# Kernel optimization log

Hardware: AMD Instinct MI355X
Metric: run time of the kernel (lower is better)

The kernel has to match this reference:

```python
import jax, jax.numpy as jnp
import numpy as np

D = 1024
H = 16
HD = D // H
COND = 128
MLP = 4 * D
B, S = 4, 1024
LN_EPS = 1e-5


def _layer_norm(x, w):
    # fp32 LayerNorm (no bias), then scale by weight, matching custom LayerNorm
    xf = x.astype(jnp.float32)
    mu = jnp.mean(xf, axis=-1, keepdims=True)
    var = jnp.mean(jnp.square(xf - mu), axis=-1, keepdims=True)
    y = (xf - mu) * jax.lax.rsqrt(var + LN_EPS)
    return y * w[None, None, :]


def _modulate(x, shift, scale):
    # shift/scale: [B, D] -> broadcast over seq
    return x * (1.0 + scale[:, None, :]) + shift[:, None, :]


def _rope(t, cos, sin):
    # t: [B,S,H,hd]; cos/sin: [S, hd//2]  (GPT-NeoX half-split rotary)
    c = cos[None, :, None, :]
    s = sin[None, :, None, :]
    t1, t2 = jnp.split(t, 2, axis=-1)
    return jnp.concatenate([t1 * c - t2 * s, t2 * c + t1 * s], axis=-1)


def setup_inputs() -> dict:
    key = jax.random.key(0)
    ks = jax.random.split(key, 12)
    std = 0.02
    inp = {
        "x": jax.random.normal(ks[0], (B, S, D), dtype=jnp.float32),
        "c": jax.random.normal(ks[1], (B, COND), dtype=jnp.float32),
        "norm1_w": jnp.ones((D,), dtype=jnp.float32),
        "norm2_w": jnp.ones((D,), dtype=jnp.float32),
        "w_qkv": jax.random.normal(ks[2], (D, 3 * D), dtype=jnp.float32) * std,
        "w_out": jax.random.normal(ks[3], (D, D), dtype=jnp.float32) * std,
        "w1": jax.random.normal(ks[4], (D, MLP), dtype=jnp.float32) * std,
        "b1": jnp.zeros((MLP,), dtype=jnp.float32),
        "w2": jax.random.normal(ks[5], (MLP, D), dtype=jnp.float32) * std,
        "b2": jnp.zeros((D,), dtype=jnp.float32),
        "adaLN_w": jax.random.normal(ks[6], (COND, 6 * D), dtype=jnp.float32) * std,
        "adaLN_b": jnp.zeros((6 * D,), dtype=jnp.float32),
    }
    # rotary tables: cos/sin [S, hd//2]
    inv_freq = 1.0 / (10000.0 ** (jnp.arange(0, HD, 2, dtype=jnp.float32) / HD))
    t = jnp.arange(S, dtype=jnp.float32)
    freqs = t[:, None] * inv_freq[None, :]  # [S, hd//2]
    inp["cos"] = jnp.cos(freqs)
    inp["sin"] = jnp.sin(freqs)
    return inp


def reference(x, c, norm1_w, norm2_w, w_qkv, w_out, w1, b1, w2, b2, adaLN_w, adaLN_b, cos, sin):
    b, s, d = x.shape
    hd = 2 * cos.shape[-1]
    h = d // hd

    # adaLN modulation -> 6 chunks of [B, D]
    mod = c @ adaLN_w + adaLN_b
    shift_msa, scale_msa, gate_msa, shift_mlp, scale_mlp, gate_mlp = jnp.split(mod, 6, axis=-1)

    x_skip = x
    xm = _modulate(_layer_norm(x, norm1_w), shift_msa, scale_msa)

    qkv = (xm @ w_qkv).reshape(b, s, 3, h, hd)
    q = _rope(qkv[:, :, 0], cos, sin)
    k = _rope(qkv[:, :, 1], cos, sin)
    v = qkv[:, :, 2]

    scale = 1.0 / jnp.sqrt(jnp.asarray(hd, dtype=x.dtype))
    scores = jnp.einsum("bshd,bthd->bhst", q, k) * scale
    probs = jax.nn.softmax(scores, axis=-1)
    attn = jnp.einsum("bhst,bthd->bshd", probs, v).reshape(b, s, d)

    # bias_dropout_add_scale (inference: dropout off): residual + gate * out
    x = x_skip + gate_msa[:, None, :] * (attn @ w_out)

    xm2 = _modulate(_layer_norm(x, norm2_w), shift_mlp, scale_mlp)
    hdn = jax.nn.gelu(xm2 @ w1 + b1, approximate=True)
    mlp_out = hdn @ w2 + b2
    x = x + gate_mlp[:, None, :] * mlp_out
    return x
```

## Files before the change

kernel.cpp:

```cpp
#include <hip/hip_runtime.h>

typedef unsigned short u16;
typedef unsigned int u32;
typedef short bf16x8 __attribute__((ext_vector_type(8)));
typedef float f32x4 __attribute__((ext_vector_type(4)));

#define DD 1024
#define SS 1024
#define HH 16
#define HDIM 64
#define MODW 6144

__device__ __forceinline__ float b2f(u16 h){ u32 u = ((u32)h)<<16; return __builtin_bit_cast(float,u); }
__device__ __forceinline__ u16 f2b(float f){
  u32 u = __builtin_bit_cast(u32,f);
  return (u16)((u + 0x7fffu + ((u>>16)&1u))>>16);
}
__device__ __forceinline__ void gload16(const u16* g, u16* l){
  __builtin_amdgcn_global_load_lds((const __attribute__((address_space(1))) void*)g,
                                   (__attribute__((address_space(3))) void*)l, 16, 0, 0);
}

__global__ void k_zero(float* __restrict__ out){
  int i = blockIdx.x*256 + threadIdx.x;
  ((float4*)out)[i] = make_float4(0.f,0.f,0.f,0.f);
}

__device__ __forceinline__ void tcast_tile(const float* in, u16* out, int K, int N, int bx, int by){
  __shared__ float t[32][33];
  int n0 = bx*32, k0 = by*32;
  int tx = threadIdx.x & 31, ty = threadIdx.x >> 5;
  #pragma unroll
  for (int i=0;i<4;i++){
    int k = k0 + ty + i*8;
    t[ty+i*8][tx] = in[(size_t)k*N + n0 + tx];
  }
  __syncthreads();
  #pragma unroll
  for (int i=0;i<4;i++){
    int n = n0 + ty + i*8;
    out[(size_t)n*K + k0 + tx] = f2b(t[tx][ty+i*8]);
  }
}
__global__ void k_prep(const float* __restrict__ wqkv, const float* __restrict__ wout,
                       const float* __restrict__ w1, const float* __restrict__ w2,
                       u16* __restrict__ wqkvT, u16* __restrict__ woutT,
                       u16* __restrict__ w1T, u16* __restrict__ w2T,
                       const float* __restrict__ c, const float* __restrict__ aw,
                       const float* __restrict__ ab, float* __restrict__ mod){
  int bid = blockIdx.x;
  if (bid < 3072)       tcast_tile(wqkv, wqkvT, 1024, 3072, bid%96,  bid/96);
  else if (bid < 4096){ int t=bid-3072; tcast_tile(wout, woutT, 1024, 1024, t%32, t/32); }
  else if (bid < 8192){ int t=bid-4096; tcast_tile(w1,   w1T,   1024, 4096, t%128,t/128); }
  else if (bid < 12288){int t=bid-8192; tcast_tile(w2,   w2T,   4096, 1024, t%32, t/32); }
  else {
    int t = bid - 12288;
    int n = (t%24)*256 + threadIdx.x;
    int bb = t/24;
    float acc = ab[n];
    #pragma unroll 4
    for (int k=0;k<128;k++) acc += c[bb*128+k]*aw[(size_t)k*MODW + n];
    mod[(size_t)bb*MODW + n] = acc;
  }
}

__global__ void k_ln_mod(const float* __restrict__ x, const float* __restrict__ w,
                         const float* __restrict__ mod, int shc, int scc,
                         u16* __restrict__ out){
  int row = blockIdx.x;
  int b = row >> 10;
  const float* xr = x + (size_t)row*DD;
  float4 v = ((const float4*)xr)[threadIdx.x];
  float s = v.x+v.y+v.z+v.w;
  float sq = v.x*v.x+v.y*v.y+v.z*v.z+v.w*v.w;
  #pragma unroll
  for (int o=32;o;o>>=1){ s += __shfl_xor(s,o); sq += __shfl_xor(sq,o); }
  __shared__ float ls[4], lq[4];
  int wid = threadIdx.x>>6, lane = threadIdx.x&63;
  if (lane==0){ ls[wid]=s; lq[wid]=sq; }
  __syncthreads();
  s = ls[0]+ls[1]+ls[2]+ls[3]; sq = lq[0]+lq[1]+lq[2]+lq[3];
  float mu = s*(1.f/DD);
  float var = sq*(1.f/DD) - mu*mu;
  float rs = rsqrtf(var + 1e-5f);
  int d0 = threadIdx.x*4;
  const float* mb = mod + (size_t)b*MODW;
  float y0 = ((v.x-mu)*rs*w[d0+0])*(1.f+mb[scc+d0+0]) + mb[shc+d0+0];
  float y1 = ((v.y-mu)*rs*w[d0+1])*(1.f+mb[scc+d0+1]) + mb[shc+d0+1];
  float y2 = ((v.z-mu)*rs*w[d0+2])*(1.f+mb[scc+d0+2]) + mb[shc+d0+2];
  float y3 = ((v.w-mu)*rs*w[d0+3])*(1.f+mb[scc+d0+3]) + mb[shc+d0+3];
  uint2 pk;
  pk.x = (u32)f2b(y0) | ((u32)f2b(y1)<<16);
  pk.y = (u32)f2b(y2) | ((u32)f2b(y3)<<16);
  ((uint2*)(out + (size_t)row*DD))[threadIdx.x] = pk;
}

enum { EPI_QKV=0, EPI_GELU=2, EPI_PARTB=5 };

template<int EPI>
__launch_bounds__(512, 2)
__global__ void k_gemm256(const u16* __restrict__ A, const u16* __restrict__ Bt,
                          int M, int N, int K, int kstride,
                          const float* __restrict__ bias,
                          u16* __restrict__ outb,
                          const float* __restrict__ cosb, const float* __restrict__ sinb,
                          u16* __restrict__ qh, u16* __restrict__ kh, u16* __restrict__ vt){
  __shared__ __align__(16) u16 lds[4][2][8192];
  int tid = threadIdx.x, lane = tid & 63;
  int wid = tid >> 6, wr = wid >> 2, wc = wid & 3;
  int bm = blockIdx.x*256, bn = blockIdx.y*256, z = blockIdx.z;
  f32x4 acc[8][4] = {};
  int srow = (tid>>6)*16 + (tid&15);
  int skk  = ((tid>>4)&3)*8;
  const u16* pa = A  + (size_t)(bm+srow)*kstride + (size_t)z*K + skk;
  const u16* pb = Bt + (size_t)(bn+srow)*kstride + (size_t)z*K + skk;
  size_t rh = (size_t)128*kstride;
  int nk = K >> 5;
  #pragma unroll
  for (int t=0; t<3; ++t){
    gload16(pa + t*32,      &lds[t][0][tid*8]);
    gload16(pa + rh + t*32, &lds[t][0][4096 + tid*8]);
    gload16(pb + t*32,      &lds[t][1][tid*8]);
    gload16(pb + rh + t*32, &lds[t][1][4096 + tid*8]);
  }
  for (int t=0; t<nk; ++t){
    const u16* lA = &lds[t&3][0][0];
    const u16* lB = &lds[t&3][1][0];
    int ahead = nk-1-t;
    if (ahead >= 2)      asm volatile("s_waitcnt vmcnt(8)" ::: "memory");
    else if (ahead == 1) asm volatile("s_waitcnt vmcnt(4)" ::: "memory");
    else                 asm volatile("s_waitcnt vmcnt(0)" ::: "memory");
    __builtin_amdgcn_s_barrier();
    if (t+3 < nk){
      int u = t+3;
      gload16(pa + u*32,      &lds[u&3][0][tid*8]);
      gload16(pa + rh + u*32, &lds[u&3][0][4096 + tid*8]);
      gload16(pb + u*32,      &lds[u&3][1][tid*8]);
      gload16(pb + rh + u*32, &lds[u&3][1][4096 + tid*8]);
    }
    bf16x8 fa[8], fb[4];
    #pragma unroll
    for (int mi=0;mi<8;mi++) fa[mi] = *(const bf16x8*)(lA + ((wr*8+mi)*64 + lane)*8);
    #pragma unroll
    for (int ni=0;ni<4;ni++) fb[ni] = *(const bf16x8*)(lB + ((wc*4+ni)*64 + lane)*8);
    asm volatile("s_waitcnt lgkmcnt(0)" ::: "memory");
    __builtin_amdgcn_sched_barrier(0);
    __builtin_amdgcn_s_setprio(1);
    #pragma unroll
    for (int mi=0;mi<8;mi++)
      #pragma unroll
      for (int ni=0;ni<4;ni++)
        acc[mi][ni] = __builtin_amdgcn_mfma_f32_16x16x32_bf16(fa[mi], fb[ni], acc[mi][ni], 0,0,0);
    __builtin_amdgcn_s_setprio(0);
  }
  int ln = lane & 15;
  int rbase = bm + wr*128 + ((lane>>4)<<2);
  if (EPI == EPI_QKV){
    int cbg = bn + wc*64;
    int ii = cbg >> 10;
    int hh = (cbg >> 6) & 15;
    if (ii == 2){
      #pragma unroll
      for (int mi=0;mi<8;mi++){
        int row = rbase + mi*16;
        int s = row & 1023, b = row >> 10;
        size_t ob = (size_t)(b*16+hh)*65536;
        #pragma unroll
        for (int ni=0;ni<4;ni++){
          int d = ni*16 + ln;
          u32 lo = (u32)f2b(acc[mi][ni][0]) | ((u32)f2b(acc[mi][ni][1])<<16);
          u32 hi = (u32)f2b(acc[mi][ni][2]) | ((u32)f2b(acc[mi][ni][3])<<16);
          *(uint2*)(vt + ob + (size_t)d*1024 + s) = make_uint2(lo,hi);
        }
      }
    } else {
      u16* dst = (ii==0) ? qh : kh;
      #pragma unroll
      for (int mi=0;mi<8;mi++){
        #pragma unroll
        for (int r=0;r<4;r++){
          int row = rbase + mi*16 + r;
          int s = row & 1023, b = row >> 10;
          size_t ob = ((size_t)(b*16+hh)*1024 + s)*64;
          #pragma unroll
          for (int ni=0;ni<2;ni++){
            int dlow = ni*16 + ln;
            float cc = cosb[s*32 + dlow], sn = sinb[s*32 + dlow];
            float t1 = acc[mi][ni][r], t2 = acc[mi][ni+2][r];
            dst[ob + dlow]      = f2b(t1*cc - t2*sn);
            dst[ob + dlow + 32] = f2b(t2*cc + t1*sn);
          }
        }
      }
    }
    return;
  }
  if (EPI == EPI_PARTB){
    u16* po = outb + (size_t)z*M*N;
    #pragma unroll
    for (int mi=0;mi<8;mi++)
      #pragma unroll
      for (int ni=0;ni<4;ni++){
        int col = bn + wc*64 + ni*16 + ln;
        #pragma unroll
        for (int r=0;r<4;r++)
          po[(size_t)(rbase+mi*16+r)*N + col] = f2b(acc[mi][ni][r]);
      }
    return;
  }
  #pragma unroll
  for (int mi=0;mi<8;mi++)
    #pragma unroll
    for (int ni=0;ni<4;ni++){
      int col = bn + wc*64 + ni*16 + ln;
      float bb = bias[col];
      #pragma unroll
      for (int r=0;r<4;r++){
        float t = acc[mi][ni][r] + bb;
        float y = 0.7978845608f*(t + 0.044715f*t*t*t);
        y = fminf(fmaxf(y, -15.f), 15.f);
        float e = __expf(2.f*y);
        float g = 0.5f*t*(1.f + (e-1.f)/(e+1.f));
        outb[(size_t)(rbase+mi*16+r)*N + col] = f2b(g);
      }
    }
}

__global__ void k_red_ln(const u16* __restrict__ part, const float* __restrict__ x,
                         const float* __restrict__ mod, const float* __restrict__ w,
                         float* __restrict__ x2, u16* __restrict__ act){
  int row = blockIdx.x;
  int b = row >> 10;
  int tid = threadIdx.x;
  int col = tid*4;
  size_t base = (size_t)row*DD + col;
  const size_t MN = (size_t)4096*1024;
  uint2 p0 = *(const uint2*)(part + base);
  uint2 p1 = *(const uint2*)(part + MN + base);
  const float* mb = mod + (size_t)b*MODW;
  float4 g = *(const float4*)(mb + 2*DD + col);
  float4 rr = *(const float4*)(x + base);
  float4 v;
  v.x = rr.x + g.x*(b2f((u16)p0.x)      + b2f((u16)p1.x));
  v.y = rr.y + g.y*(b2f((u16)(p0.x>>16))+ b2f((u16)(p1.x>>16)));
  v.z = rr.z + g.z*(b2f((u16)p0.y)      + b2f((u16)p1.y));
  v.w = rr.w + g.w*(b2f((u16)(p0.y>>16))+ b2f((u16)(p1.y>>16)));
  *(float4*)(x2 + base) = v;
  float s = v.x+v.y+v.z+v.w;
  float sq = v.x*v.x+v.y*v.y+v.z*v.z+v.w*v.w;
  #pragma unroll
  for (int o=32;o;o>>=1){ s += __shfl_xor(s,o); sq += __shfl_xor(sq,o); }
  __shared__ float ls[4], lq[4];
  int wid = tid>>6, lane = tid&63;
  if (lane==0){ ls[wid]=s; lq[wid]=sq; }
  __syncthreads();
  s = ls[0]+ls[1]+ls[2]+ls[3]; sq = lq[0]+lq[1]+lq[2]+lq[3];
  float mu = s*(1.f/DD);
  float var = sq*(1.f/DD) - mu*mu;
  float rs = rsqrtf(var + 1e-5f);
  float y0 = ((v.x-mu)*rs*w[col+0])*(1.f+mb[4*DD+col+0]) + mb[3*DD+col+0];
  float y1 = ((v.y-mu)*rs*w[col+1])*(1.f+mb[4*DD+col+1]) + mb[3*DD+col+1];
  float y2 = ((v.z-mu)*rs*w[col+2])*(1.f+mb[4*DD+col+2]) + mb[3*DD+col+2];
  float y3 = ((v.w-mu)*rs*w[col+3])*(1.f+mb[4*DD+col+3]) + mb[3*DD+col+3];
  uint2 pk;
  pk.x = (u32)f2b(y0) | ((u32)f2b(y1)<<16);
  pk.y = (u32)f2b(y2) | ((u32)f2b(y3)<<16);
  *(uint2*)(act + base) = pk;
}

__global__ void k_reduce4b(const u16* __restrict__ part, size_t MN,
                           const float* __restrict__ resid,
                           const float* __restrict__ mod, int gate_off,
                           const float* __restrict__ bias,
                           float* __restrict__ out){
  int i = blockIdx.x*256 + threadIdx.x;
  int e = i<<2;
  int col = e & 1023;
  int row = e >> 10;
  int b = row >> 10;
  float4 s = make_float4(0.f,0.f,0.f,0.f);
  #pragma unroll
  for (int z=0; z<4; z++){
    uint2 p = ((const uint2*)(part + (size_t)z*MN))[i];
    s.x += b2f((u16)p.x); s.y += b2f((u16)(p.x>>16));
    s.z += b2f((u16)p.y); s.w += b2f((u16)(p.y>>16));
  }
  float4 bb = *(const float4*)(bias + col);
  s.x+=bb.x; s.y+=bb.y; s.z+=bb.z; s.w+=bb.w;
  float4 g = *(const float4*)(mod + (size_t)b*MODW + gate_off + col);
  float4 rr = ((const float4*)resid)[i];
  float4 o;
  o.x = rr.x + g.x*s.x; o.y = rr.y + g.y*s.y;
  o.z = rr.z + g.z*s.z; o.w = rr.w + g.w*s.w;
  ((float4*)out)[i] = o;
}

__launch_bounds__(256)
__global__ void k_attn(const u16* __restrict__ qh, const u16* __restrict__ kh,
                       const u16* __restrict__ vt, u16* __restrict__ attn){
  int blk = blockIdx.x;
  int bh = blk >> 4;
  int qt = blk & 15;
  int tid = threadIdx.x, lane = tid&63, wid = tid>>6;
  int ln = lane&15, kg = lane>>4;
  __shared__ __align__(16) u16 Ks[64*72];
  __shared__ __align__(16) u16 Vs[64*72];
  __shared__ __align__(16) float ps[4][16*72];
  const size_t hb = (size_t)bh*SS*HDIM;

  int qrow = qt*64 + wid*16 + ln;
  const u16* qp = qh + hb + (size_t)qrow*64 + kg*8;
  bf16x8 qf0 = *(const bf16x8*)qp;
  bf16x8 qf1 = *(const bf16x8*)(qp + 32);

  float m[4], l[4];
  f32x4 oc[4] = {};
  #pragma unroll
  for (int r=0;r<4;r++){ m[r]=-1e30f; l[r]=0.f; }
  float* psw = ps[wid];

  for (int kt=0; kt<16; ++kt){
    __syncthreads();
    {
      int row = tid>>2, c = tid&3;
      const u16* gk = kh + hb + (size_t)(kt*64+row)*64 + c*16;
      *(uint4*)(Ks + row*72 + c*16)     = *(const uint4*)gk;
      *(uint4*)(Ks + row*72 + c*16 + 8) = *(const uint4*)(gk+8);
      const u16* gv = vt + hb + (size_t)row*1024 + kt*64 + c*16;
      *(uint4*)(Vs + row*72 + c*16)     = *(const uint4*)gv;
      *(uint4*)(Vs + row*72 + c*16 + 8) = *(const uint4*)(gv+8);
    }
    __syncthreads();

    f32x4 sc[4] = {};
    #pragma unroll
    for (int c=0;c<4;c++){
      bf16x8 kf0 = *(const bf16x8*)(Ks + (c*16+ln)*72 + kg*8);
      bf16x8 kf1 = *(const bf16x8*)(Ks + (c*16+ln)*72 + kg*8 + 32);
      sc[c] = __builtin_amdgcn_mfma_f32_16x16x32_bf16(qf0, kf0, sc[c], 0,0,0);
      sc[c] = __builtin_amdgcn_mfma_f32_16x16x32_bf16(qf1, kf1, sc[c], 0,0,0);
    }
    #pragma unroll
    for (int r=0;r<4;r++){
      float s0 = sc[0][r]*0.125f, s1 = sc[1][r]*0.125f;
      float s2 = sc[2][r]*0.125f, s3 = sc[3][r]*0.125f;
      float mx = fmaxf(fmaxf(s0,s1), fmaxf(s2,s3));
      #pragma unroll
      for (int off=8;off;off>>=1) mx = fmaxf(mx, __shfl_xor(mx, off));
      float mn = fmaxf(m[r], mx);
      float al = __expf(m[r]-mn);
      m[r] = mn;
      float p0=__expf(s0-mn), p1=__expf(s1-mn), p2=__expf(s2-mn), p3=__expf(s3-mn);
      float sum = (p0+p1)+(p2+p3);
      #pragma unroll
      for (int off=8;off;off>>=1) sum += __shfl_xor(sum, off);
      l[r] = l[r]*al + sum;
      #pragma unroll
      for (int c=0;c<4;c++) oc[c][r] *= al;
      int ro = (kg*4+r)*72;
      psw[ro +  0 + ln] = p0;
      psw[ro + 16 + ln] = p1;
      psw[ro + 32 + ln] = p2;
      psw[ro + 48 + ln] = p3;
    }
    #pragma unroll
    for (int kc=0; kc<2; ++kc){
      const float* pr = psw + ln*72 + kg*8 + kc*32;
      f32x4 a0 = *(const f32x4*)pr;
      f32x4 a1 = *(const f32x4*)(pr+4);
      bf16x8 af;
      af[0]=f2b(a0[0]); af[1]=f2b(a0[1]); af[2]=f2b(a0[2]); af[3]=f2b(a0[3]);
      af[4]=f2b(a1[0]); af[5]=f2b(a1[1]); af[6]=f2b(a1[2]); af[7]=f2b(a1[3]);
      #pragma unroll
      for (int c=0;c<4;c++){
        bf16x8 vf = *(const bf16x8*)(Vs + (c*16+ln)*72 + kg*8 + kc*32);
        oc[c] = __builtin_amdgcn_mfma_f32_16x16x32_bf16(af, vf, oc[c], 0,0,0);
      }
    }
  }
  int b = bh >> 4, h = bh & 15;
  #pragma unroll
  for (int r=0;r<4;r++){
    int srow = qt*64 + wid*16 + kg*4 + r;
    float inv = 1.f/l[r];
    u16* op = attn + (size_t)(b*1024+srow)*DD + h*64;
    #pragma unroll
    for (int c=0;c<4;c++) op[c*16+ln] = f2b(oc[c][r]*inv);
  }
}

extern "C" void kernel_launch(void* const* d_in, const int* in_sizes, int n_in,
                              void* d_out, int out_size, void* d_ws, size_t ws_size,
                              hipStream_t stream){
  const float* x   = (const float*)d_in[0];
  const float* c   = (const float*)d_in[1];
  const float* n1w = (const float*)d_in[2];
  const float* n2w = (const float*)d_in[3];
  const float* wqkv= (const float*)d_in[4];
  const float* wout= (const float*)d_in[5];
  const float* w1  = (const float*)d_in[6];
  const float* b1  = (const float*)d_in[7];
  const float* w2  = (const float*)d_in[8];
  const float* b2  = (const float*)d_in[9];
  const float* aw  = (const float*)d_in[10];
  const float* ab  = (const float*)d_in[11];
  const float* cosb= (const float*)d_in[12];
  const float* sinb= (const float*)d_in[13];

  const size_t REQ = 117538816;
  if (ws_size < REQ){
    k_zero<<<4096,256,0,stream>>>((float*)d_out);
    return;
  }
  char* ws = (char*)d_ws;
  u16*   wqkvT = (u16*)(ws + 0);
  u16*   woutT = (u16*)(ws + 6291456);
  u16*   act   = (u16*)(ws + 8388608);
  float* mod   = (float*)(ws + 16777216);
  float* x2    = (float*)(ws + 16875520);
  u16*   qh    = (u16*)(ws + 16875520);
  u16*   kh    = (u16*)(ws + 25264128);
  u16*   vt    = (u16*)(ws + 33652736);
  u16*   part2b= (u16*)(ws + 33652736);
  u16*   hbuf  = (u16*)(ws + 33652736);
  u16*   w1T   = (u16*)(ws + 67207168);
  u16*   w2T   = (u16*)(ws + 75595776);
  u16*   part4b= (u16*)(ws + 83984384);

  k_prep<<<12384,256,0,stream>>>(wqkv, wout, w1, w2, wqkvT, woutT, w1T, w2T, c, aw, ab, mod);
  k_ln_mod<<<4096,256,0,stream>>>(x, n1w, mod, 0*DD, 1*DD, act);
  k_gemm256<EPI_QKV ><<<dim3(16,12,1),512,0,stream>>>(act, wqkvT, 4096,3072,1024,1024,
        nullptr, nullptr, cosb, sinb, qh, kh, vt);
  k_attn<<<1024,256,0,stream>>>(qh, kh, vt, act);
  k_gemm256<EPI_PARTB><<<dim3(16,4,2),512,0,stream>>>(act, woutT, 4096,1024,512,1024,
        nullptr, part2b, nullptr, nullptr, nullptr, nullptr, nullptr);
  k_red_ln<<<4096,256,0,stream>>>(part2b, x, mod, n2w, x2, act);
  k_gemm256<EPI_GELU><<<dim3(16,16,1),512,0,stream>>>(act, w1T, 4096,4096,1024,1024,
        b1, hbuf, nullptr, nullptr, nullptr, nullptr, nullptr);
  k_gemm256<EPI_PARTB><<<dim3(16,4,4),512,0,stream>>>(hbuf, w2T, 4096,1024,1024,4096,
        nullptr, part4b, nullptr, nullptr, nullptr, nullptr, nullptr);
  k_reduce4b<<<4096,256,0,stream>>>(part4b, (size_t)4096*1024, x2, mod, 5*DD, b2, (float*)d_out);
}
```

Baseline: 377.5 us.

## Double-buffer attention K/V via async LDS loads and keep P in registers

Rewrites the attention inner loop to prefetch the next K/V tile into a second LDS buffer using global_load_lds with XOR-swizzled layout, overlapping loads with compute. The QK^T operands are swapped so each lane owns a query column, which removes the per-row shuffle reductions and the fp32 LDS round trip for probabilities. P is packed to bf16 with the hardware pack-convert instruction and redistributed by shuffles instead. The softmax scale is folded into Q in the QKV epilogue, and the attention kernel now requests an occupancy hint. This adds shuffle traffic and hand-placed waitcnt/barrier logic that must stay correct.

```diff
diff --git a/kernel.cpp b/kernel.cpp
--- a/kernel.cpp
+++ b/kernel.cpp
@@ -15,6 +15,9 @@
 __device__ __forceinline__ u16 f2b(float f){
   u32 u = __builtin_bit_cast(u32,f);
   return (u16)((u + 0x7fffu + ((u>>16)&1u))>>16);
+}
+__device__ __forceinline__ u32 cvtpk(float a, float b){
+  u32 r; asm("v_cvt_pk_bf16_f32 %0, %1, %2" : "=v"(r) : "v"(a), "v"(b)); return r;
 }
 __device__ __forceinline__ void gload16(const u16* g, u16* l){
   __builtin_amdgcn_global_load_lds((const __attribute__((address_space(1))) void*)g,
@@ -175,6 +178,7 @@
       }
     } else {
       u16* dst = (ii==0) ? qh : kh;
+      float qs = (ii==0) ? 0.125f : 1.0f;
       #pragma unroll
       for (int mi=0;mi<8;mi++){
         #pragma unroll
@@ -187,8 +191,8 @@
             int dlow = ni*16 + ln;
             float cc = cosb[s*32 + dlow], sn = sinb[s*32 + dlow];
             float t1 = acc[mi][ni][r], t2 = acc[mi][ni+2][r];
-            dst[ob + dlow]      = f2b(t1*cc - t2*sn);
-            dst[ob + dlow + 32] = f2b(t2*cc + t1*sn);
+            dst[ob + dlow]      = f2b((t1*cc - t2*sn)*qs);
+            dst[ob + dlow + 32] = f2b((t2*cc + t1*sn)*qs);
           }
         }
       }
@@ -295,7 +299,7 @@
   ((float4*)out)[i] = o;
 }
 
-__launch_bounds__(256)
+__launch_bounds__(256, 4)
 __global__ void k_attn(const u16* __restrict__ qh, const u16* __restrict__ kh,
                        const u16* __restrict__ vt, u16* __restrict__ attn){
   int blk = blockIdx.x;
@@ -303,9 +307,8 @@
   int qt = blk & 15;
   int tid = threadIdx.x, lane = tid&63, wid = tid>>6;
   int ln = lane&15, kg = lane>>4;
-  __shared__ __align__(16) u16 Ks[64*72];
-  __shared__ __align__(16) u16 Vs[64*72];
-  __shared__ __align__(16) float ps[4][16*72];
+  int sw = ln & 7;
+  __shared__ __align__(16) u16 KV[2][2][4096];
   const size_t hb = (size_t)bh*SS*HDIM;
 
   int qrow = qt*64 + wid*16 + ln;
@@ -313,79 +316,105 @@
   bf16x8 qf0 = *(const bf16x8*)qp;
   bf16x8 qf1 = *(const bf16x8*)(qp + 32);
 
-  float m[4], l[4];
+  int w0i = wid*64 + lane, w1i = w0i + 256;
+  int r0 = w0i>>3, sl0 = (w0i&7) ^ (r0&7);
+  int r1 = w1i>>3, sl1 = (w1i&7) ^ (r1&7);
+  const u16* gk0 = kh + hb + (size_t)r0*64 + sl0*8;
+  const u16* gk1 = kh + hb + (size_t)r1*64 + sl1*8;
+  const u16* gv0 = vt + hb + (size_t)r0*1024 + sl0*8;
+  const u16* gv1 = vt + hb + (size_t)r1*1024 + sl1*8;
+
+  float mrun = -1e30f, lrun = 0.f;
   f32x4 oc[4] = {};
-  #pragma unroll
-  for (int r=0;r<4;r++){ m[r]=-1e30f; l[r]=0.f; }
-  float* psw = ps[wid];
+
+  gload16(gk0, &KV[0][0][w0i*8]);
+  gload16(gk1, &KV[0][0][w1i*8]);
+  gload16(gv0, &KV[0][1][w0i*8]);
+  gload16(gv1, &KV[0][1][w1i*8]);
 
   for (int kt=0; kt<16; ++kt){
-    __syncthreads();
-    {
-      int row = tid>>2, c = tid&3;
-      const u16* gk = kh + hb + (size_t)(kt*64+row)*64 + c*16;
-      *(uint4*)(Ks + row*72 + c*16)     = *(const uint4*)gk;
-      *(uint4*)(Ks + row*72 + c*16 + 8) = *(const uint4*)(gk+8);
-      const u16* gv = vt + hb + (size_t)row*1024 + kt*64 + c*16;
-      *(uint4*)(Vs + row*72 + c*16)     = *(const uint4*)gv;
-      *(uint4*)(Vs + row*72 + c*16 + 8) = *(const uint4*)(gv+8);
-    }
-    __syncthreads();
-
-    f32x4 sc[4] = {};
+    int buf = kt & 1;
+    __builtin_amdgcn_s_barrier();
+    asm volatile("" ::: "memory");
+    if (kt < 15){
+      int u = kt+1;
+      gload16(gk0 + u*4096, &KV[buf^1][0][w0i*8]);
+      gload16(gk1 + u*4096, &KV[buf^1][0][w1i*8]);
+      gload16(gv0 + u*64,   &KV[buf^1][1][w0i*8]);
+      gload16(gv1 + u*64,   &KV[buf^1][1][w1i*8]);
+      asm volatile("s_waitcnt vmcnt(4)" ::: "memory");
+    } else {
+      asm volatile("s_waitcnt vmcnt(0)" ::: "memory");
+    }
+    __builtin_amdgcn_s_barrier();
+    const u16* Kb = KV[buf][0];
+    const u16* Vb = KV[buf][1];
+
+    f32x4 sc[4];
     #pragma unroll
     for (int c=0;c<4;c++){
-      bf16x8 kf0 = *(const bf16x8*)(Ks + (c*16+ln)*72 + kg*8);
-      bf16x8 kf1 = *(const bf16x8*)(Ks + (c*16+ln)*72 + kg*8 + 32);
-      sc[c] = __builtin_amdgcn_mfma_f32_16x16x32_bf16(qf0, kf0, sc[c], 0,0,0);
-      sc[c] = __builtin_amdgcn_mfma_f32_16x16x32_bf16(qf1, kf1, sc[c], 0,0,0);
-    }
-    #pragma unroll
-    for (int r=0;r<4;r++){
-      float s0 = sc[0][r]*0.125f, s1 = sc[1][r]*0.125f;
-      float s2 = sc[2][r]*0.125f, s3 = sc[3][r]*0.125f;
-      float mx = fmaxf(fmaxf(s0,s1), fmaxf(s2,s3));
-      #pragma unroll
-      for (int off=8;off;off>>=1) mx = fmaxf(mx, __shfl_xor(mx, off));
-      float mn = fmaxf(m[r], mx);
-      float al = __expf(m[r]-mn);
-      m[r] = mn;
-      float p0=__expf(s0-mn), p1=__expf(s1-mn), p2=__expf(s2-mn), p3=__expf(s3-mn);
-      float sum = (p0+p1)+(p2+p3);
-      #pragma unroll
-      for (int off=8;off;off>>=1) sum += __shfl_xor(sum, off);
-      l[r] = l[r]*al + sum;
-      #pragma unroll
-      for (int c=0;c<4;c++) oc[c][r] *= al;
-      int ro = (kg*4+r)*72;
-      psw[ro +  0 + ln] = p0;
-      psw[ro + 16 + ln] = p1;
-      psw[ro + 32 + ln] = p2;
-      psw[ro + 48 + ln] = p3;
-    }
-    #pragma unroll
-    for (int kc=0; kc<2; ++kc){
-      const float* pr = psw + ln*72 + kg*8 + kc*32;
-      f32x4 a0 = *(const f32x4*)pr;
-      f32x4 a1 = *(const f32x4*)(pr+4);
-      bf16x8 af;
-      af[0]=f2b(a0[0]); af[1]=f2b(a0[1]); af[2]=f2b(a0[2]); af[3]=f2b(a0[3]);
-      af[4]=f2b(a1[0]); af[5]=f2b(a1[1]); af[6]=f2b(a1[2]); af[7]=f2b(a1[3]);
+      const u16* kr = Kb + (c*16+ln)*64;
+      bf16x8 kf0 = *(const bf16x8*)(kr + (((kg  )^sw)<<3));
+      bf16x8 kf1 = *(const bf16x8*)(kr + (((kg+4)^sw)<<3));
+      f32x4 zz = {};
+      zz   = __builtin_amdgcn_mfma_f32_16x16x32_bf16(kf0, qf0, zz, 0,0,0);
+      sc[c]= __builtin_amdgcn_mfma_f32_16x16x32_bf16(kf1, qf1, zz, 0,0,0);
+    }
+    float mx = fmaxf(fmaxf(fmaxf(sc[0][0],sc[0][1]),fmaxf(sc[0][2],sc[0][3])),
+                     fmaxf(fmaxf(sc[1][0],sc[1][1]),fmaxf(sc[1][2],sc[1][3])));
+    float mx2= fmaxf(fmaxf(fmaxf(sc[2][0],sc[2][1]),fmaxf(sc[2][2],sc[2][3])),
+                     fmaxf(fmaxf(sc[3][0],sc[3][1]),fmaxf(sc[3][2],sc[3][3])));
+    mx = fmaxf(mx, mx2);
+    mx = fmaxf(mx, __shfl_xor(mx, 16));
+    mx = fmaxf(mx, __shfl_xor(mx, 32));
+    float mn = fmaxf(mrun, mx);
+    float al = __expf(mrun - mn);
+    mrun = mn;
+    u32 pk[4][2];
+    float sum = 0.f;
+    #pragma unroll
+    for (int c=0;c<4;c++){
+      float p0 = __expf(sc[c][0]-mn), p1 = __expf(sc[c][1]-mn);
+      float p2 = __expf(sc[c][2]-mn), p3 = __expf(sc[c][3]-mn);
+      sum += (p0+p1)+(p2+p3);
+      pk[c][0] = cvtpk(p0,p1);
+      pk[c][1] = cvtpk(p2,p3);
+    }
+    sum += __shfl_xor(sum, 16);
+    sum += __shfl_xor(sum, 32);
+    lrun = lrun*al + sum;
+    float alr0 = __shfl(al, kg*4+0), alr1 = __shfl(al, kg*4+1);
+    float alr2 = __shfl(al, kg*4+2), alr3 = __shfl(al, kg*4+3);
+    #pragma unroll
+    for (int c=0;c<4;c++){ oc[c][0]*=alr0; oc[c][1]*=alr1; oc[c][2]*=alr2; oc[c][3]*=alr3; }
+    int srcA = ((kg&1)<<5) + ln;
+    int hi = kg >> 1;
+    #pragma unroll
+    for (int kc=0;kc<2;kc++){
+      u32 a0 = (u32)__shfl((int)pk[2*kc  ][0], srcA   ), b0 = (u32)__shfl((int)pk[2*kc+1][0], srcA   );
+      u32 a1 = (u32)__shfl((int)pk[2*kc  ][1], srcA   ), b1 = (u32)__shfl((int)pk[2*kc+1][1], srcA   );
+      u32 a2 = (u32)__shfl((int)pk[2*kc  ][0], srcA+16), b2 = (u32)__shfl((int)pk[2*kc+1][0], srcA+16);
+      u32 a3 = (u32)__shfl((int)pk[2*kc  ][1], srcA+16), b3 = (u32)__shfl((int)pk[2*kc+1][1], srcA+16);
+      uint4 wv = make_uint4(hi? b0:a0, hi? b1:a1, hi? b2:a2, hi? b3:a3);
+      bf16x8 af = __builtin_bit_cast(bf16x8, wv);
       #pragma unroll
       for (int c=0;c<4;c++){
-        bf16x8 vf = *(const bf16x8*)(Vs + (c*16+ln)*72 + kg*8 + kc*32);
+        const u16* vr = Vb + (c*16+ln)*64;
+        bf16x8 vf = *(const bf16x8*)(vr + (((kg+4*kc)^sw)<<3));
         oc[c] = __builtin_amdgcn_mfma_f32_16x16x32_bf16(af, vf, oc[c], 0,0,0);
       }
     }
   }
   int b = bh >> 4, h = bh & 15;
+  float linv[4];
+  linv[0] = 1.f/__shfl(lrun, kg*4+0); linv[1] = 1.f/__shfl(lrun, kg*4+1);
+  linv[2] = 1.f/__shfl(lrun, kg*4+2); linv[3] = 1.f/__shfl(lrun, kg*4+3);
   #pragma unroll
   for (int r=0;r<4;r++){
     int srow = qt*64 + wid*16 + kg*4 + r;
-    float inv = 1.f/l[r];
     u16* op = attn + (size_t)(b*1024+srow)*DD + h*64;
     #pragma unroll
-    for (int c=0;c<4;c++) op[c*16+ln] = f2b(oc[c][r]*inv);
+    for (int c=0;c<4;c++) op[c*16+ln] = f2b(oc[c][r]*linv[r]);
   }
 }
 
```

Result: faster. 351.5 us (-6.9%).
